# Performance work log

Measured on AMD Instinct MI355X. Metric: run time of the kernel, lower is better.

## Reference

```python
import jax, jax.numpy as jnp
import numpy as np
from jax import lax

B, R, F = 100, 15, 4096       # batch, regions, feature dim
V, E, D, A, T = 10000, 1024, 1024, 512, 500  # vocab, embed, decoder, attention, topic
LIN = 1024                    # autoencoder linear output width
NT = 5                        # sentences per paragraph
L = 52                        # max caption length


def setup_inputs() -> dict:
    key = jax.random.key(0)
    ks = jax.random.split(key, 16)
    g = lambda i, shp, s: jax.random.normal(ks[i], shp, jnp.float32) * s
    return {
        "image_features": g(0, (B, R, F), 1.0),
        "encoded_captions": jax.random.randint(ks[1], (B, NT, L), 0, V),
        "caption_lengths": jax.random.randint(ks[2], (B, NT), 1, L),
        # autoencoder
        "W_lt": g(3, (LIN, F), 0.02), "b_lt": jnp.zeros((LIN,), jnp.float32),
        "conv_w": g(4, (6, 1, 15, 26), 0.05), "conv_b": jnp.zeros((6,), jnp.float32),
        # attention MLP (weight_norm linears == plain linears mathematically)
        "W_feat": g(5, (A, F), 0.02), "b_feat": jnp.zeros((A,), jnp.float32),
        "W_dec": g(6, (A, D), 0.02), "b_dec": jnp.zeros((A,), jnp.float32),
        "W_top": g(7, (A, T), 0.02), "b_top": jnp.zeros((A,), jnp.float32),
        "W_full": g(8, (1, A), 0.02), "b_full": jnp.zeros((1,), jnp.float32),
        # embedding + LSTM cells + output heads
        "emb": g(9, (V, E), 0.1),
        "W_ih1": g(10, (4 * D, E + F + D), 0.01), "W_hh1": g(11, (4 * D, D), 0.01),
        "b_ih1": jnp.zeros((4 * D,), jnp.float32), "b_hh1": jnp.zeros((4 * D,), jnp.float32),
        "W_ih2": g(12, (4 * D, F + D), 0.01), "W_hh2": g(13, (4 * D, D), 0.01),
        "b_ih2": jnp.zeros((4 * D,), jnp.float32), "b_hh2": jnp.zeros((4 * D,), jnp.float32),
        "W_fc1": g(14, (V, D), 0.02), "b_fc1": jnp.zeros((V,), jnp.float32),
        "W_fc": g(15, (V, D), 0.02), "b_fc": jnp.zeros((V,), jnp.float32),
    }


def _lstm_cell(x, h, c, W_ih, W_hh, b_ih, b_hh):
    gates = x @ W_ih.T + b_ih + h @ W_hh.T + b_hh
    i, f, g_, o = jnp.split(gates, 4, axis=-1)
    c = jax.nn.sigmoid(f) * c + jax.nn.sigmoid(i) * jnp.tanh(g_)
    h = jax.nn.sigmoid(o) * jnp.tanh(c)
    return h, c


def reference(image_features, encoded_captions, caption_lengths, W_lt, b_lt,
              conv_w, conv_b, W_feat, b_feat, W_dec, b_dec, W_top, b_top,
              W_full, b_full, emb, W_ih1, W_hh1, b_ih1, b_hh1,
              W_ih2, W_hh2, b_ih2, b_hh2, W_fc1, b_fc1, W_fc, b_fc):
    def per_sample(img, caps, lens):
        # img (R,F), caps (NT,L) int, lens (NT,) int
        img_mean = img.mean(0)  # (F,)
        # autoencoder: linear 4096->1024, conv2d(1->6, k=(15,26), stride 2)
        x = (img @ W_lt.T + b_lt)[None, None]  # (1,1,R,LIN)
        conv = lax.conv_general_dilated(x, conv_w, (2, 2), "VALID",
                                        dimension_numbers=("NCHW", "OIHW", "NCHW"))
        topics = conv[0, :, 0, :] + conv_b[:, None]  # (6, T=500)
        att1 = img @ W_feat.T + b_feat               # (R,A), precomputed once
        # last word of each sentence: caps[t, lens[t]-1]
        last_words = jnp.take_along_axis(caps, (lens - 1)[:, None], axis=1)[:, 0]  # (NT,)
        last_embs = emb[last_words]                  # (NT,E)

        def step(carry, tup):
            h1, c1, h2, c2 = carry
            topic_t, emb_t = tup
            # top-down attention LSTM: cat([h2, img_mean, word_emb])
            x1 = jnp.concatenate([h2, img_mean, emb_t])
            h1, c1 = _lstm_cell(x1, h1, c1, W_ih1, W_hh1, b_ih1, b_hh1)
            # attention over R regions (dropout is identity in eval)
            att = jax.nn.relu(att1 + (h1 @ W_dec.T + b_dec) + (topic_t @ W_top.T + b_top))
            scores = att @ W_full[0] + b_full[0]     # (R,)
            alpha = jax.nn.softmax(scores)
            awe = alpha @ img                        # (F,)
            preds1 = h1 @ W_fc1.T + b_fc1            # (V,)
            h2, c2 = _lstm_cell(jnp.concatenate([awe, h1]), h2, c2,
                                W_ih2, W_hh2, b_ih2, b_hh2)
            preds = h2 @ W_fc.T + b_fc               # (V,)
            return (h1, c1, h2, c2), (preds, preds1)

        z = jnp.zeros((D,), img.dtype)
        _, (preds, preds1) = lax.scan(step, (z, z, z, z), (topics[:NT], last_embs))
        return preds, preds1                          # (NT,V) each

    preds, preds1 = jax.vmap(per_sample)(image_features, encoded_captions, caption_lengths)
    return preds, preds1, encoded_captions, caption_lengths - 1
```

## Files before the change

kernel.cpp:

```cpp
#include <hip/hip_runtime.h>

typedef __attribute__((ext_vector_type(8))) short short8;
typedef __attribute__((ext_vector_type(4))) short short4v;
typedef __attribute__((ext_vector_type(4))) float f32x4;

__device__ __forceinline__ unsigned short f2bf(float f) {
  unsigned int u = __float_as_uint(f);
  u += 0x7fffu + ((u >> 16) & 1u);
  return (unsigned short)(u >> 16);
}
__device__ __forceinline__ float bf2f(unsigned short u) {
  return __uint_as_float(((unsigned int)u) << 16);
}
__device__ __forceinline__ float sigm(float x) { return 1.f / (1.f + expf(-x)); }

template<int NKC>
__global__ __launch_bounds__(256) void gemm_v5(
    const unsigned short* __restrict__ X, int ldx,
    const unsigned short* __restrict__ W, int ldw, int N,
    unsigned short* __restrict__ C, long long slotStride)
{
  __shared__ short8 lds[3584];
  const int tid = threadIdx.x;
  const int lane = tid & 63, wv = tid >> 6;
  const int l16 = lane & 15, kg = (lane >> 4) * 8;
  const int mbase = blockIdx.y * 112;
  const int ncol = blockIdx.x * 64 + wv * 16 + l16;
  const int nrow = (ncol < N) ? ncol : (N - 1);
  const long long k0 = (long long)blockIdx.z * (NKC * 256);
  C += (long long)blockIdx.z * slotStride;

  const unsigned short* wp = W + (size_t)nrow * ldw + kg + k0;
  const unsigned short* xb = X + (size_t)(mbase + l16) * ldx + kg + k0;
  const size_t xrow = (size_t)16 * ldx;

  f32x4 acc[7];
#pragma unroll
  for (int i = 0; i < 7; ++i) acc[i] = (f32x4){0.f, 0.f, 0.f, 0.f};

  for (int kc = 0; kc < NKC; ++kc) {
    if (kc) __syncthreads();
    short8 wbuf[8];
#pragma unroll
    for (int ks = 0; ks < 8; ++ks)
      wbuf[ks] = *(const short8*)(wp + kc * 256 + ks * 32);
    short8 xst[14];
#pragma unroll
    for (int i = 0; i < 14; ++i) {
      const int f = wv + i * 4, mt = f >> 3, ks = f & 7;
      xst[i] = *(const short8*)(xb + (size_t)mt * xrow + kc * 256 + ks * 32);
    }
#pragma unroll
    for (int i = 0; i < 14; ++i) lds[(wv + i * 4) * 64 + lane] = xst[i];
    __syncthreads();
#pragma unroll
    for (int ks = 0; ks < 8; ++ks)
#pragma unroll
      for (int mt = 0; mt < 7; ++mt) {
        short8 a = lds[(mt * 8 + ks) * 64 + lane];
        acc[mt] = __builtin_amdgcn_mfma_f32_16x16x32_bf16(a, wbuf[ks], acc[mt], 0, 0, 0);
      }
  }
  if (ncol < N) {
    const int r0 = (lane >> 4) * 4;
#pragma unroll
    for (int mt = 0; mt < 7; ++mt)
#pragma unroll
      for (int r = 0; r < 4; ++r)
        C[(size_t)(mbase + mt * 16 + r0 + r) * N + ncol] = f2bf(acc[mt][r]);
  }
}

template<int NKC>
__global__ __launch_bounds__(256) void gemm_v5f(
    const unsigned short* __restrict__ X, int ldx,
    const float* __restrict__ W, int ldw, int N,
    unsigned short* __restrict__ C, long long slotStride)
{
  __shared__ short8 lds[3584];
  const int tid = threadIdx.x;
  const int lane = tid & 63, wv = tid >> 6;
  const int l16 = lane & 15, kg = (lane >> 4) * 8;
  const int mbase = blockIdx.y * 112;
  const int ncol = blockIdx.x * 64 + wv * 16 + l16;
  const int nrow = (ncol < N) ? ncol : (N - 1);
  const long long k0 = (long long)blockIdx.z * (NKC * 256);
  C += (long long)blockIdx.z * slotStride;

  const float* wp = W + (size_t)nrow * ldw + kg + k0;
  const unsigned short* xb = X + (size_t)(mbase + l16) * ldx + kg + k0;
  const size_t xrow = (size_t)16 * ldx;

  f32x4 acc[7];
#pragma unroll
  for (int i = 0; i < 7; ++i) acc[i] = (f32x4){0.f, 0.f, 0.f, 0.f};

  for (int kc = 0; kc < NKC; ++kc) {
    if (kc) __syncthreads();
    float4 wa[8], wb[8];
#pragma unroll
    for (int ks = 0; ks < 8; ++ks) {
      wa[ks] = *(const float4*)(wp + kc * 256 + ks * 32);
      wb[ks] = *(const float4*)(wp + kc * 256 + ks * 32 + 4);
    }
    short8 xst[14];
#pragma unroll
    for (int i = 0; i < 14; ++i) {
      const int f = wv + i * 4, mt = f >> 3, ks = f & 7;
      xst[i] = *(const short8*)(xb + (size_t)mt * xrow + kc * 256 + ks * 32);
    }
#pragma unroll
    for (int i = 0; i < 14; ++i) lds[(wv + i * 4) * 64 + lane] = xst[i];
    __syncthreads();
#pragma unroll
    for (int ks = 0; ks < 8; ++ks) {
      short8 w;
      w[0] = (short)f2bf(wa[ks].x); w[1] = (short)f2bf(wa[ks].y);
      w[2] = (short)f2bf(wa[ks].z); w[3] = (short)f2bf(wa[ks].w);
      w[4] = (short)f2bf(wb[ks].x); w[5] = (short)f2bf(wb[ks].y);
      w[6] = (short)f2bf(wb[ks].z); w[7] = (short)f2bf(wb[ks].w);
#pragma unroll
      for (int mt = 0; mt < 7; ++mt) {
        short8 a = lds[(mt * 8 + ks) * 64 + lane];
        acc[mt] = __builtin_amdgcn_mfma_f32_16x16x32_bf16(a, w, acc[mt], 0, 0, 0);
      }
    }
  }
  if (ncol < N) {
    const int r0 = (lane >> 4) * 4;
#pragma unroll
    for (int mt = 0; mt < 7; ++mt)
#pragma unroll
      for (int r = 0; r < 4; ++r)
        C[(size_t)(mbase + mt * 16 + r0 + r) * N + ncol] = f2bf(acc[mt][r]);
  }
}

template<int NKC>
__global__ __launch_bounds__(256) void gemm_dwf(
    const unsigned short* __restrict__ X, int ldx,
    const float* __restrict__ W, int ldw, int N,
    float* __restrict__ outF, const float* __restrict__ bias,
    long long ldc, int rowLim)
{
  __shared__ short8 lds[3584];
  const int tid = threadIdx.x;
  const int lane = tid & 63, wv = tid >> 6;
  const int l16 = lane & 15, kg = (lane >> 4) * 8;
  const int mbase = blockIdx.y * 112;
  const int ncol = blockIdx.x * 64 + wv * 16 + l16;
  const int nrow = (ncol < N) ? ncol : (N - 1);

  const float* wp = W + (size_t)nrow * ldw + kg;
  const unsigned short* xb = X + (size_t)(mbase + l16) * ldx + kg;
  const size_t xrow = (size_t)16 * ldx;

  f32x4 acc[7];
#pragma unroll
  for (int i = 0; i < 7; ++i) acc[i] = (f32x4){0.f, 0.f, 0.f, 0.f};

  for (int kc = 0; kc < NKC; ++kc) {
    if (kc) __syncthreads();
    float4 wa[8], wb[8];
#pragma unroll
    for (int ks = 0; ks < 8; ++ks) {
      wa[ks] = *(const float4*)(wp + kc * 256 + ks * 32);
      wb[ks] = *(const float4*)(wp + kc * 256 + ks * 32 + 4);
    }
    short8 xst[14];
#pragma unroll
    for (int i = 0; i < 14; ++i) {
      const int f = wv + i * 4, mt = f >> 3, ks = f & 7;
      xst[i] = *(const short8*)(xb + (size_t)mt * xrow + kc * 256 + ks * 32);
    }
#pragma unroll
    for (int i = 0; i < 14; ++i) lds[(wv + i * 4) * 64 + lane] = xst[i];
    __syncthreads();
#pragma unroll
    for (int ks = 0; ks < 8; ++ks) {
      short8 w;
      w[0] = (short)f2bf(wa[ks].x); w[1] = (short)f2bf(wa[ks].y);
      w[2] = (short)f2bf(wa[ks].z); w[3] = (short)f2bf(wa[ks].w);
      w[4] = (short)f2bf(wb[ks].x); w[5] = (short)f2bf(wb[ks].y);
      w[6] = (short)f2bf(wb[ks].z); w[7] = (short)f2bf(wb[ks].w);
#pragma unroll
      for (int mt = 0; mt < 7; ++mt) {
        short8 a = lds[(mt * 8 + ks) * 64 + lane];
        acc[mt] = __builtin_amdgcn_mfma_f32_16x16x32_bf16(a, w, acc[mt], 0, 0, 0);
      }
    }
  }
  if (ncol < N) {
    const float bv = bias ? bias[ncol] : 0.f;
    const int r0 = (lane >> 4) * 4;
#pragma unroll
    for (int mt = 0; mt < 7; ++mt)
#pragma unroll
      for (int r = 0; r < 4; ++r) {
        const int row = mbase + mt * 16 + r0 + r;
        if (row < rowLim) outF[(size_t)row * ldc + ncol] = acc[mt][r] + bv;
      }
  }
}

template<int NKC>
__global__ __launch_bounds__(256) void gemm_dwf_split(
    const unsigned short* __restrict__ X, int ldx,
    const float* __restrict__ W1, const float* __restrict__ W2,
    float* __restrict__ outF, const float* __restrict__ bias,
    unsigned short* __restrict__ aux)
{
  __shared__ short8 lds[3584];
  const int tid = threadIdx.x;
  const int lane = tid & 63, wv = tid >> 6;
  const int l16 = lane & 15, kg = (lane >> 4) * 8;
  const int ncol0 = blockIdx.x * 64 + wv * 16 + l16;
  const int ncol = (ncol0 < 10512) ? ncol0 : 10511;
  const float* wp = ((ncol < 10000) ? W1 + (size_t)ncol * 1024
                                    : W2 + (size_t)(ncol - 10000) * 1024) + kg;
  const unsigned short* xb = X + (size_t)l16 * ldx + kg;
  const size_t xrow = (size_t)16 * ldx;

  f32x4 acc[7];
#pragma unroll
  for (int i = 0; i < 7; ++i) acc[i] = (f32x4){0.f, 0.f, 0.f, 0.f};

  for (int kc = 0; kc < NKC; ++kc) {
    if (kc) __syncthreads();
    float4 wa[8], wb[8];
#pragma unroll
    for (int ks = 0; ks < 8; ++ks) {
      wa[ks] = *(const float4*)(wp + kc * 256 + ks * 32);
      wb[ks] = *(const float4*)(wp + kc * 256 + ks * 32 + 4);
    }
    short8 xst[14];
#pragma unroll
    for (int i = 0; i < 14; ++i) {
      const int f = wv + i * 4, mt = f >> 3, ks = f & 7;
      xst[i] = *(const short8*)(xb + (size_t)mt * xrow + kc * 256 + ks * 32);
    }
#pragma unroll
    for (int i = 0; i < 14; ++i) lds[(wv + i * 4) * 64 + lane] = xst[i];
    __syncthreads();
#pragma unroll
    for (int ks = 0; ks < 8; ++ks) {
      short8 w;
      w[0] = (short)f2bf(wa[ks].x); w[1] = (short)f2bf(wa[ks].y);
      w[2] = (short)f2bf(wa[ks].z); w[3] = (short)f2bf(wa[ks].w);
      w[4] = (short)f2bf(wb[ks].x); w[5] = (short)f2bf(wb[ks].y);
      w[6] = (short)f2bf(wb[ks].z); w[7] = (short)f2bf(wb[ks].w);
#pragma unroll
      for (int mt = 0; mt < 7; ++mt) {
        short8 a = lds[(mt * 8 + ks) * 64 + lane];
        acc[mt] = __builtin_amdgcn_mfma_f32_16x16x32_bf16(a, w, acc[mt], 0, 0, 0);
      }
    }
  }
  if (ncol0 < 10000) {
    const float bv = bias[ncol0];
    const int r0 = (lane >> 4) * 4;
#pragma unroll
    for (int mt = 0; mt < 7; ++mt)
#pragma unroll
      for (int r = 0; r < 4; ++r) {
        const int row = mt * 16 + r0 + r;
        if (row < 100) outF[(size_t)row * 50000 + ncol0] = acc[mt][r] + bv;
      }
  } else if (ncol0 < 10512) {
    const int r0 = (lane >> 4) * 4;
#pragma unroll
    for (int mt = 0; mt < 7; ++mt)
#pragma unroll
      for (int r = 0; r < 4; ++r)
        aux[(size_t)(mt * 16 + r0 + r) * 512 + (ncol0 - 10000)] = f2bf(acc[mt][r]);
  }
}

__global__ __launch_bounds__(256) void k_pack_all(
    const float* __restrict__ Wih1, const float* __restrict__ Whh1,
    const float* __restrict__ Wih2, const float* __restrict__ Whh2,
    const float* __restrict__ Wtop,
    unsigned short* __restrict__ Wg1, unsigned short* __restrict__ Wg2,
    unsigned short* __restrict__ Wtopb)
{
  int i = blockIdx.x * 256 + threadIdx.x;
  float4 v; unsigned short* dst; long long di;
  if (i < 2097152) {
    int row = i >> 9, c4 = i & 511;
    const float* s = (c4 < 256) ? Wih1 + (size_t)row * 6144 + c4 * 4
                                : Whh1 + (size_t)row * 1024 + (c4 - 256) * 4;
    v = *(const float4*)s; dst = Wg1; di = i;
  } else if (i < 8388608) {
    int j = i - 2097152; int row = j / 1536, c4 = j - row * 1536;
    const float* s = (c4 < 1280) ? Wih2 + (size_t)row * 5120 + c4 * 4
                                 : Whh2 + (size_t)row * 1024 + (c4 - 1280) * 4;
    v = *(const float4*)s; dst = Wg2; di = j;
  } else {
    int j = i - 8388608; if (j >= 65536) return;
    int n = j >> 7, c4 = j & 127;
    v = (c4 < 125) ? *(const float4*)(Wtop + (size_t)n * 500 + c4 * 4)
                   : (float4){0.f, 0.f, 0.f, 0.f};
    dst = Wtopb; di = j;
  }
  short4v o; o[0] = (short)f2bf(v.x); o[1] = (short)f2bf(v.y);
  o[2] = (short)f2bf(v.z); o[3] = (short)f2bf(v.w);
  ((short4v*)dst)[di] = o;
}

__global__ __launch_bounds__(256) void k_ximg2(const float* __restrict__ img,
    unsigned short* __restrict__ Ximg, unsigned short* __restrict__ Xmean) {
  int idx = blockIdx.x * 256 + threadIdx.x;
  int b = idx >> 12, f = idx & 4095;
  float s = 0.f;
#pragma unroll
  for (int r = 0; r < 15; ++r) {
    float v = img[((size_t)(b * 15 + r) << 12) + f];
    s += v;
    Ximg[((size_t)(b * 15 + r) << 12) + f] = f2bf(v);
  }
  Xmean[((size_t)b << 12) + f] = f2bf(s * (1.f / 15.f));
}

__global__ __launch_bounds__(512) void k_conv(const float* __restrict__ lin,
    const float* __restrict__ cw, const float* __restrict__ cb,
    float* __restrict__ topics) {
  int b = blockIdx.x;
  __shared__ float L[15 * 1024];
  for (int i = threadIdx.x; i < 15 * 1024; i += 512) L[i] = lin[(size_t)b * 15360 + i];
  __syncthreads();
  for (int idx = threadIdx.x; idx < 2500; idx += 512) {
    int tt = idx / 500, w = idx - tt * 500;
    float s = cb[tt];
    for (int kh = 0; kh < 15; ++kh) {
      const float* lr = &L[kh * 1024 + 2 * w];
      const float* wr = &cw[(tt * 15 + kh) * 26];
#pragma unroll
      for (int kw = 0; kw < 26; ++kw) s += lr[kw] * wr[kw];
    }
    topics[(size_t)b * 2500 + idx] = s;
  }
}

__global__ __launch_bounds__(256) void k_padtop(const float* __restrict__ topics,
    unsigned short* __restrict__ Xtop) {
  int idx = blockIdx.x * 256 + threadIdx.x;
  if (idx >= 560 * 512) return;
  int r = idx >> 9, k = idx & 511;
  Xtop[idx] = (r < 500 && k < 500) ? f2bf(topics[(size_t)r * 500 + k]) : (unsigned short)0;
}

__global__ void k_wc(const int* __restrict__ caps, const int* __restrict__ lens,
                     int* __restrict__ words, float* __restrict__ out2,
                     float* __restrict__ out3) {
  int idx = blockIdx.x * 256 + threadIdx.x;
  if (idx < 26000) out2[idx] = (float)caps[idx];
  if (idx < 500) {
    int len = lens[idx];
    words[idx] = caps[idx * 52 + len - 1];
    out3[idx] = (float)(len - 1);
  }
}

__global__ __launch_bounds__(256) void k_gather(const float* __restrict__ emb,
    const int* __restrict__ words, unsigned short* __restrict__ Xemb) {
  int idx = blockIdx.x * 256 + threadIdx.x;
  int bt = idx >> 10, e = idx & 1023;
  Xemb[idx] = (bt < 500) ? f2bf(emb[(size_t)words[bt] * 1024 + e]) : (unsigned short)0;
}

__global__ __launch_bounds__(256) void k_gbase1(const unsigned short* __restrict__ P,
    const float* __restrict__ bih, const float* __restrict__ bhh,
    float* __restrict__ gb) {
  int idx = blockIdx.x * 256 + threadIdx.x;
  int m = idx >> 12, n = idx & 4095;
  float s = bih[n] + bhh[n];
#pragma unroll
  for (int sl = 0; sl < 4; ++sl) s += bf2f(P[((size_t)sl * 112 + m) * 4096 + n]);
  gb[idx] = s;
}

__global__ __launch_bounds__(256) void k_lstm1(const unsigned short* __restrict__ P,
    const float* __restrict__ gb1, const float* __restrict__ gemb, int t,
    float* __restrict__ c1, unsigned short* __restrict__ Xh1,
    unsigned short* __restrict__ X1, unsigned short* __restrict__ X2) {
  int idx = blockIdx.x * 256 + threadIdx.x;
  int b = idx >> 10, j = idx & 1023;
  float g[4];
#pragma unroll
  for (int x = 0; x < 4; ++x) {
    int col = (x << 10) + j;
    float s = gb1[b * 4096 + col] + gemb[((size_t)b * 5 + t) * 4096 + col];
#pragma unroll
    for (int sl = 0; sl < 4; ++sl) s += bf2f(P[((size_t)sl * 112 + b) * 4096 + col]);
    g[x] = s;
  }
  float c = sigm(g[1]) * c1[idx] + sigm(g[0]) * tanhf(g[2]);
  float h = sigm(g[3]) * tanhf(c);
  c1[idx] = c;
  unsigned short hb = f2bf(h);
  Xh1[idx] = hb;
  X1[b * 2048 + 1024 + j] = hb;
  X2[(size_t)b * 6144 + 4096 + j] = hb;
}

__global__ __launch_bounds__(256) void k_attawe(const float* __restrict__ att1,
    const unsigned short* __restrict__ padec, const float* __restrict__ bdec,
    const float* __restrict__ btop, const unsigned short* __restrict__ ttopb,
    const float* __restrict__ wfull, int t,
    const unsigned short* __restrict__ Ximg, unsigned short* __restrict__ X2) {
  int b = blockIdx.x;
  int tid = threadIdx.x;
  int r = tid & 15, ch = tid >> 4;
  __shared__ float sp[16][17];
  __shared__ float al[16];
  float s = 0.f;
  if (r < 15) {
    const float* a1 = att1 + ((size_t)b * 15 + r) * 512;
    const unsigned short* tp = ttopb + ((size_t)b * 5 + t) * 512;
#pragma unroll
    for (int j = 0; j < 32; ++j) {
      int n = ch * 32 + j;
      float ad = bdec[n] + btop[n] + bf2f(padec[(size_t)b * 512 + n]);
      float v = a1[n] + ad + bf2f(tp[n]);
      s += fmaxf(v, 0.f) * wfull[n];
    }
  }
  sp[r][ch] = s;
  __syncthreads();
  if (tid == 0) {
    float sc[15];
    float m = -1e30f;
    for (int rr = 0; rr < 15; ++rr) {
      float x = 0.f;
      for (int cc = 0; cc < 16; ++cc) x += sp[rr][cc];
      sc[rr] = x; m = fmaxf(m, x);
    }
    float sum = 0.f;
    for (int rr = 0; rr < 15; ++rr) { sc[rr] = expf(sc[rr] - m); sum += sc[rr]; }
    float inv = 1.f / sum;
    for (int rr = 0; rr < 15; ++rr) al[rr] = sc[rr] * inv;
  }
  __syncthreads();
  for (int f = tid; f < 4096; f += 256) {
    float s2 = 0.f;
#pragma unroll
    for (int rr = 0; rr < 15; ++rr)
      s2 += al[rr] * bf2f(Ximg[((size_t)b * 15 + rr) * 4096 + f]);
    X2[(size_t)b * 6144 + f] = f2bf(s2);
  }
}

__global__ __launch_bounds__(256) void k_lstm2(const unsigned short* __restrict__ P,
    const float* __restrict__ bih, const float* __restrict__ bhh,
    float* __restrict__ c2, unsigned short* __restrict__ Xh2,
    unsigned short* __restrict__ X1, unsigned short* __restrict__ X2) {
  int idx = blockIdx.x * 256 + threadIdx.x;
  int b = idx >> 10, j = idx & 1023;
  float g[4];
#pragma unroll
  for (int x = 0; x < 4; ++x) {
    int col = (x << 10) + j;
    float s = bih[col] + bhh[col];
#pragma unroll
    for (int sl = 0; sl < 6; ++sl) s += bf2f(P[((size_t)sl * 112 + b) * 4096 + col]);
    g[x] = s;
  }
  float c = sigm(g[1]) * c2[idx] + sigm(g[0]) * tanhf(g[2]);
  float h = sigm(g[3]) * tanhf(c);
  c2[idx] = c;
  unsigned short hb = f2bf(h);
  Xh2[idx] = hb;
  X1[b * 2048 + j] = hb;
  X2[(size_t)b * 6144 + 5120 + j] = hb;
}

extern "C" void kernel_launch(void* const* d_in, const int* in_sizes, int n_in,
                              void* d_out, int out_size, void* d_ws, size_t ws_size,
                              hipStream_t stream) {
  (void)in_sizes; (void)n_in; (void)out_size;
  const float* imgf  = (const float*)d_in[0];
  const int*   caps  = (const int*)d_in[1];
  const int*   lens  = (const int*)d_in[2];
  const float* W_lt  = (const float*)d_in[3];
  const float* b_lt  = (const float*)d_in[4];
  const float* convw = (const float*)d_in[5];
  const float* convb = (const float*)d_in[6];
  const float* W_feat = (const float*)d_in[7];
  const float* b_feat = (const float*)d_in[8];
  const float* W_dec = (const float*)d_in[9];
  const float* b_dec = (const float*)d_in[10];
  const float* W_top = (const float*)d_in[11];
  const float* b_top = (const float*)d_in[12];
  const float* W_full = (const float*)d_in[13];
  const float* b_full = (const float*)d_in[14];  (void)b_full;
  const float* emb   = (const float*)d_in[15];
  const float* W_ih1 = (const float*)d_in[16];
  const float* W_hh1 = (const float*)d_in[17];
  const float* b_ih1 = (const float*)d_in[18];
  const float* b_hh1 = (const float*)d_in[19];
  const float* W_ih2 = (const float*)d_in[20];
  const float* W_hh2 = (const float*)d_in[21];
  const float* b_ih2 = (const float*)d_in[22];
  const float* b_hh2 = (const float*)d_in[23];
  const float* W_fc1 = (const float*)d_in[24];
  const float* b_fc1 = (const float*)d_in[25];
  const float* W_fc  = (const float*)d_in[26];
  const float* b_fc  = (const float*)d_in[27];
  float* out = (float*)d_out;

  char* ws = (char*)d_ws;
  size_t off = 0;
  auto alloc = [&](size_t bytes) -> size_t {
    size_t o = off; off = (off + bytes + 255) & ~(size_t)255; return o;
  };
  const size_t oZERO  = off;
  const size_t oXimg  = alloc(1568ull * 4096 * 2);
  const size_t oXmean = alloc(112ull * 4096 * 2);
  const size_t oX1    = alloc(112ull * 2048 * 2);
  const size_t oX2    = alloc(112ull * 6144 * 2);
  const size_t oXh1   = alloc(112ull * 1024 * 2);
  const size_t oXh2   = alloc(112ull * 1024 * 2);
  const size_t oc1    = alloc(100ull * 1024 * 4);
  const size_t oc2    = alloc(100ull * 1024 * 4);
  const size_t zeroBytes = off - oZERO;
  const size_t oXemb  = alloc(560ull * 1024 * 2);
  const size_t olin   = alloc(1568ull * 1024 * 4);
  const size_t otop   = alloc(100ull * 2500 * 4);
  const size_t oXtop  = alloc(560ull * 512 * 2);
  const size_t oTtopb = alloc(560ull * 512 * 2);
  const size_t oatt1  = alloc(1568ull * 512 * 4);
  const size_t ogb1   = alloc(112ull * 4096 * 4);
  const size_t ogemb  = alloc(560ull * 4096 * 4);
  const size_t owords = alloc(512ull * 4);
  const size_t opg    = alloc(6ull * 112 * 4096 * 2);
  const size_t opadec = alloc(112ull * 512 * 2);
  const size_t oWg1   = alloc(4096ull * 2048 * 2);
  const size_t oWg2   = alloc(4096ull * 6144 * 2);
  const size_t oWtopb = alloc(512ull * 512 * 2);
  if (ws_size < off) return;

  unsigned short* Ximg  = (unsigned short*)(ws + oXimg);
  unsigned short* Xmean = (unsigned short*)(ws + oXmean);
  unsigned short* Xemb  = (unsigned short*)(ws + oXemb);
  unsigned short* X1    = (unsigned short*)(ws + oX1);
  unsigned short* X2    = (unsigned short*)(ws + oX2);
  unsigned short* Xh1   = (unsigned short*)(ws + oXh1);
  unsigned short* Xh2   = (unsigned short*)(ws + oXh2);
  float* c1    = (float*)(ws + oc1);
  float* c2    = (float*)(ws + oc2);
  float* lin   = (float*)(ws + olin);
  float* topics = (float*)(ws + otop);
  unsigned short* Xtop  = (unsigned short*)(ws + oXtop);
  unsigned short* Ttopb = (unsigned short*)(ws + oTtopb);
  float* att1  = (float*)(ws + oatt1);
  float* gb1   = (float*)(ws + ogb1);
  float* gemb  = (float*)(ws + ogemb);
  int*   words = (int*)(ws + owords);
  unsigned short* pg    = (unsigned short*)(ws + opg);
  unsigned short* padec = (unsigned short*)(ws + opadec);
  unsigned short* Wg1   = (unsigned short*)(ws + oWg1);
  unsigned short* Wg2   = (unsigned short*)(ws + oWg2);
  unsigned short* Wtopb = (unsigned short*)(ws + oWtopb);

  const long long S4 = 112ll * 4096;

  hipMemsetAsync(ws + oZERO, 0, zeroBytes, stream);

  k_ximg2<<<1600, 256, 0, stream>>>(imgf, Ximg, Xmean);
  k_pack_all<<<33024, 256, 0, stream>>>(W_ih1, W_hh1, W_ih2, W_hh2, W_top,
                                        Wg1, Wg2, Wtopb);
  gemm_dwf<16><<<dim3(16, 14, 1), 256, 0, stream>>>(Ximg, 4096, W_lt, 4096, 1024,
                                                    lin, b_lt, 1024, 1568);
  k_conv<<<100, 512, 0, stream>>>(lin, convw, convb, topics);
  k_padtop<<<1120, 256, 0, stream>>>(topics, Xtop);
  gemm_v5<2><<<dim3(8, 5, 1), 256, 0, stream>>>(Xtop, 512, Wtopb, 512, 512, Ttopb, 0);
  gemm_dwf<16><<<dim3(8, 14, 1), 256, 0, stream>>>(Ximg, 4096, W_feat, 4096, 512,
                                                   att1, b_feat, 512, 1568);
  k_wc<<<102, 256, 0, stream>>>(caps, lens, words, out + 10000000, out + 10026000);
  k_gather<<<2240, 256, 0, stream>>>(emb, words, Xemb);
  gemm_v5f<4><<<dim3(64, 1, 4), 256, 0, stream>>>(Xmean, 4096, W_ih1 + 1024, 6144, 4096,
                                                  pg, S4);
  k_gbase1<<<1792, 256, 0, stream>>>(pg, b_ih1, b_hh1, gb1);
  gemm_dwf<4><<<dim3(64, 5, 1), 256, 0, stream>>>(Xemb, 1024, W_ih1 + 5120, 6144, 4096,
                                                  gemb, nullptr, 4096, 560);

  for (int t = 0; t < 5; ++t) {
    gemm_v5<2><<<dim3(64, 1, 4), 256, 0, stream>>>(X1, 2048, Wg1, 2048, 4096, pg, S4);
    k_lstm1<<<400, 256, 0, stream>>>(pg, gb1, gemb, t, c1, Xh1, X1, X2);
    gemm_dwf_split<4><<<dim3(165, 1, 1), 256, 0, stream>>>(
        Xh1, 1024, W_fc1, W_dec, out + 5000000 + t * 10000, b_fc1, padec);
    k_attawe<<<100, 256, 0, stream>>>(att1, padec, b_dec, b_top, Ttopb, W_full, t,
                                      Ximg, X2);
    gemm_v5<4><<<dim3(64, 1, 6), 256, 0, stream>>>(X2, 6144, Wg2, 6144, 4096, pg, S4);
    k_lstm2<<<400, 256, 0, stream>>>(pg, b_ih2, b_hh2, c2, Xh2, X1, X2);
    gemm_dwf<4><<<dim3(157, 1, 1), 256, 0, stream>>>(Xh2, 1024, W_fc, 1024, 10000,
                                                     out + t * 10000, b_fc, 50000, 100);
  }
}
```

Baseline: 789.2 us.

## Double-buffer GEMMs with direct global-to-LDS loads, prepack fc weights to bf16, split-K prologue

Replaces all GEMM kernels with double-buffered variants that use global_load_lds to stage X and W tiles into shared memory, overlapping the next chunk's loads with MFMA compute. W_fc1/W_dec and W_fc are pre-packed to bf16 once so the per-step output heads read half the bytes and skip per-element conversion. Prologue GEMMs (W_lt, W_feat) move to split-K with bf16 partials plus a reduce kernel, and several small kernels (padtop, wc/gather) are fused into conv and a new gather kernel. This adds extra packing traffic and larger LDS usage, which may reduce occupancy, and split-K partials in bf16 add rounding.

```diff
diff --git a/kernel.cpp b/kernel.cpp
--- a/kernel.cpp
+++ b/kernel.cpp
@@ -14,251 +14,245 @@
 }
 __device__ __forceinline__ float sigm(float x) { return 1.f / (1.f + expf(-x)); }
 
-template<int NKC>
-__global__ __launch_bounds__(256) void gemm_v5(
+typedef const __attribute__((address_space(1))) unsigned int GUI;
+typedef __attribute__((address_space(3))) unsigned int LUI;
+__device__ __forceinline__ void g2l16(const void* g, void* l) {
+  __builtin_amdgcn_global_load_lds((GUI*)g, (LUI*)l, 16, 0, 0);
+}
+template<int N> __device__ __forceinline__ void waitvm() {
+  if constexpr (N == 0)       asm volatile("s_waitcnt vmcnt(0)" ::: "memory");
+  else if constexpr (N == 11) asm volatile("s_waitcnt vmcnt(11)" ::: "memory");
+  else                        asm volatile("s_waitcnt vmcnt(15)" ::: "memory");
+}
+
+template<int NCH, bool OUTF32>
+__global__ __launch_bounds__(256) void gemm_pb(
     const unsigned short* __restrict__ X, int ldx,
     const unsigned short* __restrict__ W, int ldw, int N,
-    unsigned short* __restrict__ C, long long slotStride)
+    void* __restrict__ Cv, long long slotStride,
+    const float* __restrict__ bias, long long ldc, int rowLim)
 {
-  __shared__ short8 lds[3584];
-  const int tid = threadIdx.x;
-  const int lane = tid & 63, wv = tid >> 6;
+  __shared__ __align__(16) char smem[2 * 28672 + 2 * 16384];
+  const int tid = threadIdx.x, lane = tid & 63, wv = tid >> 6;
   const int l16 = lane & 15, kg = (lane >> 4) * 8;
   const int mbase = blockIdx.y * 112;
   const int ncol = blockIdx.x * 64 + wv * 16 + l16;
   const int nrow = (ncol < N) ? ncol : (N - 1);
-  const long long k0 = (long long)blockIdx.z * (NKC * 256);
-  C += (long long)blockIdx.z * slotStride;
-
-  const unsigned short* wp = W + (size_t)nrow * ldw + kg + k0;
-  const unsigned short* xb = X + (size_t)(mbase + l16) * ldx + kg + k0;
-  const size_t xrow = (size_t)16 * ldx;
+  const long long kbase = (long long)blockIdx.z * (NCH * 128);
+
+  const unsigned short* xb = X + (size_t)(mbase + l16) * ldx + kbase + kg;
+  const unsigned short* wb = W + (size_t)nrow * ldw + kbase + kg;
+  const size_t xrow16 = (size_t)16 * ldx;
+
+  auto stage = [&](int nb, int ch) {
+#pragma unroll
+    for (int i = 0; i < 7; ++i) {
+      const int f = wv + i * 4, mt = f >> 2, ks = f & 3;
+      g2l16(xb + (size_t)mt * xrow16 + ch * 128 + ks * 32,
+            smem + nb * 28672 + f * 1024);
+    }
+#pragma unroll
+    for (int ks = 0; ks < 4; ++ks)
+      g2l16(wb + ch * 128 + ks * 32,
+            smem + 57344 + nb * 16384 + (wv * 4 + ks) * 1024);
+  };
 
   f32x4 acc[7];
 #pragma unroll
   for (int i = 0; i < 7; ++i) acc[i] = (f32x4){0.f, 0.f, 0.f, 0.f};
 
-  for (int kc = 0; kc < NKC; ++kc) {
-    if (kc) __syncthreads();
-    short8 wbuf[8];
-#pragma unroll
-    for (int ks = 0; ks < 8; ++ks)
-      wbuf[ks] = *(const short8*)(wp + kc * 256 + ks * 32);
-    short8 xst[14];
-#pragma unroll
-    for (int i = 0; i < 14; ++i) {
-      const int f = wv + i * 4, mt = f >> 3, ks = f & 7;
-      xst[i] = *(const short8*)(xb + (size_t)mt * xrow + kc * 256 + ks * 32);
-    }
-#pragma unroll
-    for (int i = 0; i < 14; ++i) lds[(wv + i * 4) * 64 + lane] = xst[i];
-    __syncthreads();
-#pragma unroll
-    for (int ks = 0; ks < 8; ++ks)
+  stage(0, 0);
+#pragma unroll
+  for (int t = 0; t < NCH; ++t) {
+    if (t + 1 < NCH) { stage((t + 1) & 1, t + 1); waitvm<11>(); }
+    else waitvm<0>();
+    __builtin_amdgcn_s_barrier();
+    __builtin_amdgcn_sched_barrier(0);
+    const char* xs  = smem + (t & 1) * 28672;
+    const char* wsm = smem + 57344 + (t & 1) * 16384;
+#pragma unroll
+    for (int ks = 0; ks < 4; ++ks) {
+      short8 w = *(const short8*)(wsm + (wv * 4 + ks) * 1024 + lane * 16);
 #pragma unroll
       for (int mt = 0; mt < 7; ++mt) {
-        short8 a = lds[(mt * 8 + ks) * 64 + lane];
-        acc[mt] = __builtin_amdgcn_mfma_f32_16x16x32_bf16(a, wbuf[ks], acc[mt], 0, 0, 0);
+        short8 a = *(const short8*)(xs + (mt * 4 + ks) * 1024 + lane * 16);
+        acc[mt] = __builtin_amdgcn_mfma_f32_16x16x32_bf16(a, w, acc[mt], 0, 0, 0);
       }
-  }
+    }
+    __builtin_amdgcn_sched_barrier(0);
+    __builtin_amdgcn_s_barrier();
+  }
+
   if (ncol < N) {
     const int r0 = (lane >> 4) * 4;
-#pragma unroll
-    for (int mt = 0; mt < 7; ++mt)
-#pragma unroll
-      for (int r = 0; r < 4; ++r)
-        C[(size_t)(mbase + mt * 16 + r0 + r) * N + ncol] = f2bf(acc[mt][r]);
-  }
-}
-
-template<int NKC>
-__global__ __launch_bounds__(256) void gemm_v5f(
+    if constexpr (OUTF32) {
+      float* outF = (float*)Cv;
+      const float bv = bias ? bias[ncol] : 0.f;
+#pragma unroll
+      for (int mt = 0; mt < 7; ++mt)
+#pragma unroll
+        for (int r = 0; r < 4; ++r) {
+          const int row = mbase + mt * 16 + r0 + r;
+          if (row < rowLim) outF[(size_t)row * ldc + ncol] = acc[mt][r] + bv;
+        }
+    } else {
+      unsigned short* C = (unsigned short*)Cv + (long long)blockIdx.z * slotStride;
+#pragma unroll
+      for (int mt = 0; mt < 7; ++mt)
+#pragma unroll
+        for (int r = 0; r < 4; ++r)
+          C[(size_t)(mbase + mt * 16 + r0 + r) * N + ncol] = f2bf(acc[mt][r]);
+    }
+  }
+}
+
+template<int NCH, bool OUTF32>
+__global__ __launch_bounds__(256) void gemm_pf(
     const unsigned short* __restrict__ X, int ldx,
     const float* __restrict__ W, int ldw, int N,
-    unsigned short* __restrict__ C, long long slotStride)
+    void* __restrict__ Cv, long long slotStride,
+    const float* __restrict__ bias, long long ldc, int rowLim)
 {
-  __shared__ short8 lds[3584];
-  const int tid = threadIdx.x;
-  const int lane = tid & 63, wv = tid >> 6;
+  __shared__ __align__(16) char smem[2 * 28672 + 2 * 32768];
+  const int tid = threadIdx.x, lane = tid & 63, wv = tid >> 6;
   const int l16 = lane & 15, kg = (lane >> 4) * 8;
   const int mbase = blockIdx.y * 112;
   const int ncol = blockIdx.x * 64 + wv * 16 + l16;
   const int nrow = (ncol < N) ? ncol : (N - 1);
-  const long long k0 = (long long)blockIdx.z * (NKC * 256);
-  C += (long long)blockIdx.z * slotStride;
-
-  const float* wp = W + (size_t)nrow * ldw + kg + k0;
-  const unsigned short* xb = X + (size_t)(mbase + l16) * ldx + kg + k0;
-  const size_t xrow = (size_t)16 * ldx;
+  const long long kbase = (long long)blockIdx.z * (NCH * 128);
+
+  const unsigned short* xb = X + (size_t)(mbase + l16) * ldx + kbase + kg;
+  const float* wb = W + (size_t)nrow * ldw + kbase + kg;
+  const size_t xrow16 = (size_t)16 * ldx;
+
+  auto stage = [&](int nb, int ch) {
+#pragma unroll
+    for (int i = 0; i < 7; ++i) {
+      const int f = wv + i * 4, mt = f >> 2, ks = f & 3;
+      g2l16(xb + (size_t)mt * xrow16 + ch * 128 + ks * 32,
+            smem + nb * 28672 + f * 1024);
+    }
+#pragma unroll
+    for (int ks = 0; ks < 4; ++ks)
+#pragma unroll
+      for (int h = 0; h < 2; ++h)
+        g2l16(wb + ch * 128 + ks * 32 + h * 4,
+              smem + 57344 + nb * 32768 + ((wv * 4 + ks) * 2 + h) * 1024);
+  };
 
   f32x4 acc[7];
 #pragma unroll
   for (int i = 0; i < 7; ++i) acc[i] = (f32x4){0.f, 0.f, 0.f, 0.f};
 
-  for (int kc = 0; kc < NKC; ++kc) {
-    if (kc) __syncthreads();
-    float4 wa[8], wb[8];
-#pragma unroll
-    for (int ks = 0; ks < 8; ++ks) {
-      wa[ks] = *(const float4*)(wp + kc * 256 + ks * 32);
-      wb[ks] = *(const float4*)(wp + kc * 256 + ks * 32 + 4);
-    }
-    short8 xst[14];
-#pragma unroll
-    for (int i = 0; i < 14; ++i) {
-      const int f = wv + i * 4, mt = f >> 3, ks = f & 7;
-      xst[i] = *(const short8*)(xb + (size_t)mt * xrow + kc * 256 + ks * 32);
-    }
-#pragma unroll
-    for (int i = 0; i < 14; ++i) lds[(wv + i * 4) * 64 + lane] = xst[i];
-    __syncthreads();
-#pragma unroll
-    for (int ks = 0; ks < 8; ++ks) {
+  stage(0, 0);
+#pragma unroll
+  for (int t = 0; t < NCH; ++t) {
+    if (t + 1 < NCH) { stage((t + 1) & 1, t + 1); waitvm<15>(); }
+    else waitvm<0>();
+    __builtin_amdgcn_s_barrier();
+    __builtin_amdgcn_sched_barrier(0);
+    const char* xs  = smem + (t & 1) * 28672;
+    const char* wsm = smem + 57344 + (t & 1) * 32768;
+#pragma unroll
+    for (int ks = 0; ks < 4; ++ks) {
+      float4 wa = *(const float4*)(wsm + ((wv * 4 + ks) * 2 + 0) * 1024 + lane * 16);
+      float4 wc = *(const float4*)(wsm + ((wv * 4 + ks) * 2 + 1) * 1024 + lane * 16);
       short8 w;
-      w[0] = (short)f2bf(wa[ks].x); w[1] = (short)f2bf(wa[ks].y);
-      w[2] = (short)f2bf(wa[ks].z); w[3] = (short)f2bf(wa[ks].w);
-      w[4] = (short)f2bf(wb[ks].x); w[5] = (short)f2bf(wb[ks].y);
-      w[6] = (short)f2bf(wb[ks].z); w[7] = (short)f2bf(wb[ks].w);
+      w[0] = (short)f2bf(wa.x); w[1] = (short)f2bf(wa.y);
+      w[2] = (short)f2bf(wa.z); w[3] = (short)f2bf(wa.w);
+      w[4] = (short)f2bf(wc.x); w[5] = (short)f2bf(wc.y);
+      w[6] = (short)f2bf(wc.z); w[7] = (short)f2bf(wc.w);
 #pragma unroll
       for (int mt = 0; mt < 7; ++mt) {
-        short8 a = lds[(mt * 8 + ks) * 64 + lane];
+        short8 a = *(const short8*)(xs + (mt * 4 + ks) * 1024 + lane * 16);
         acc[mt] = __builtin_amdgcn_mfma_f32_16x16x32_bf16(a, w, acc[mt], 0, 0, 0);
       }
     }
-  }
+    __builtin_amdgcn_sched_barrier(0);
+    __builtin_amdgcn_s_barrier();
+  }
+
   if (ncol < N) {
     const int r0 = (lane >> 4) * 4;
-#pragma unroll
-    for (int mt = 0; mt < 7; ++mt)
-#pragma unroll
-      for (int r = 0; r < 4; ++r)
-        C[(size_t)(mbase + mt * 16 + r0 + r) * N + ncol] = f2bf(acc[mt][r]);
-  }
-}
-
-template<int NKC>
-__global__ __launch_bounds__(256) void gemm_dwf(
-    const unsigned short* __restrict__ X, int ldx,
-    const float* __restrict__ W, int ldw, int N,
+    if constexpr (OUTF32) {
+      float* outF = (float*)Cv;
+      const float bv = bias ? bias[ncol] : 0.f;
+#pragma unroll
+      for (int mt = 0; mt < 7; ++mt)
+#pragma unroll
+        for (int r = 0; r < 4; ++r) {
+          const int row = mbase + mt * 16 + r0 + r;
+          if (row < rowLim) outF[(size_t)row * ldc + ncol] = acc[mt][r] + bv;
+        }
+    } else {
+      unsigned short* C = (unsigned short*)Cv + (long long)blockIdx.z * slotStride;
+#pragma unroll
+      for (int mt = 0; mt < 7; ++mt)
+#pragma unroll
+        for (int r = 0; r < 4; ++r)
+          C[(size_t)(mbase + mt * 16 + r0 + r) * N + ncol] = f2bf(acc[mt][r]);
+    }
+  }
+}
+
+__global__ __launch_bounds__(256) void gemm_pcat(
+    const unsigned short* __restrict__ X,
+    const unsigned short* __restrict__ W,
     float* __restrict__ outF, const float* __restrict__ bias,
-    long long ldc, int rowLim)
+    unsigned short* __restrict__ padec)
 {
-  __shared__ short8 lds[3584];
-  const int tid = threadIdx.x;
-  const int lane = tid & 63, wv = tid >> 6;
+  __shared__ __align__(16) char smem[2 * 28672 + 2 * 16384];
+  const int tid = threadIdx.x, lane = tid & 63, wv = tid >> 6;
   const int l16 = lane & 15, kg = (lane >> 4) * 8;
-  const int mbase = blockIdx.y * 112;
-  const int ncol = blockIdx.x * 64 + wv * 16 + l16;
-  const int nrow = (ncol < N) ? ncol : (N - 1);
-
-  const float* wp = W + (size_t)nrow * ldw + kg;
-  const unsigned short* xb = X + (size_t)(mbase + l16) * ldx + kg;
-  const size_t xrow = (size_t)16 * ldx;
+  const int ncol0 = blockIdx.x * 64 + wv * 16 + l16;
+  const int nrow = (ncol0 < 10512) ? ncol0 : 10511;
+
+  const unsigned short* xb = X + (size_t)l16 * 1024 + kg;
+  const unsigned short* wb = W + (size_t)nrow * 1024 + kg;
+  const size_t xrow16 = (size_t)16 * 1024;
+
+  auto stage = [&](int nb, int ch) {
+#pragma unroll
+    for (int i = 0; i < 7; ++i) {
+      const int f = wv + i * 4, mt = f >> 2, ks = f & 3;
+      g2l16(xb + (size_t)mt * xrow16 + ch * 128 + ks * 32,
+            smem + nb * 28672 + f * 1024);
+    }
+#pragma unroll
+    for (int ks = 0; ks < 4; ++ks)
+      g2l16(wb + ch * 128 + ks * 32,
+            smem + 57344 + nb * 16384 + (wv * 4 + ks) * 1024);
+  };
 
   f32x4 acc[7];
 #pragma unroll
   for (int i = 0; i < 7; ++i) acc[i] = (f32x4){0.f, 0.f, 0.f, 0.f};
 
-  for (int kc = 0; kc < NKC; ++kc) {
-    if (kc) __syncthreads();
-    float4 wa[8], wb[8];
-#pragma unroll
-    for (int ks = 0; ks < 8; ++ks) {
-      wa[ks] = *(const float4*)(wp + kc * 256 + ks * 32);
-      wb[ks] = *(const float4*)(wp + kc * 256 + ks * 32 + 4);
-    }
-    short8 xst[14];
-#pragma unroll
-    for (int i = 0; i < 14; ++i) {
-      const int f = wv + i * 4, mt = f >> 3, ks = f & 7;
-      xst[i] = *(const short8*)(xb + (size_t)mt * xrow + kc * 256 + ks * 32);
-    }
-#pragma unroll
-    for (int i = 0; i < 14; ++i) lds[(wv + i * 4) * 64 + lane] = xst[i];
-    __syncthreads();
-#pragma unroll
-    for (int ks = 0; ks < 8; ++ks) {
-      short8 w;
-      w[0] = (short)f2bf(wa[ks].x); w[1] = (short)f2bf(wa[ks].y);
-      w[2] = (short)f2bf(wa[ks].z); w[3] = (short)f2bf(wa[ks].w);
-      w[4] = (short)f2bf(wb[ks].x); w[5] = (short)f2bf(wb[ks].y);
-      w[6] = (short)f2bf(wb[ks].z); w[7] = (short)f2bf(wb[ks].w);
+  stage(0, 0);
+#pragma unroll
+  for (int t = 0; t < 8; ++t) {
+    if (t + 1 < 8) { stage((t + 1) & 1, t + 1); waitvm<11>(); }
+    else waitvm<0>();
+    __builtin_amdgcn_s_barrier();
+    __builtin_amdgcn_sched_barrier(0);
+    const char* xs  = smem + (t & 1) * 28672;
+    const char* wsm = smem + 57344 + (t & 1) * 16384;
+#pragma unroll
+    for (int ks = 0; ks < 4; ++ks) {
+      short8 w = *(const short8*)(wsm + (wv * 4 + ks) * 1024 + lane * 16);
 #pragma unroll
       for (int mt = 0; mt < 7; ++mt) {
-        short8 a = lds[(mt * 8 + ks) * 64 + lane];
+        short8 a = *(const short8*)(xs + (mt * 4 + ks) * 1024 + lane * 16);
         acc[mt] = __builtin_amdgcn_mfma_f32_16x16x32_bf16(a, w, acc[mt], 0, 0, 0);
       }
     }
-  }
-  if (ncol < N) {
-    const float bv = bias ? bias[ncol] : 0.f;
-    const int r0 = (lane >> 4) * 4;
-#pragma unroll
-    for (int mt = 0; mt < 7; ++mt)
-#pragma unroll
-      for (int r = 0; r < 4; ++r) {
-        const int row = mbase + mt * 16 + r0 + r;
-        if (row < rowLim) outF[(size_t)row * ldc + ncol] = acc[mt][r] + bv;
-      }
-  }
-}
-
-template<int NKC>
-__global__ __launch_bounds__(256) void gemm_dwf_split(
-    const unsigned short* __restrict__ X, int ldx,
-    const float* __restrict__ W1, const float* __restrict__ W2,
-    float* __restrict__ outF, const float* __restrict__ bias,
-    unsigned short* __restrict__ aux)
-{
-  __shared__ short8 lds[3584];
-  const int tid = threadIdx.x;
-  const int lane = tid & 63, wv = tid >> 6;
-  const int l16 = lane & 15, kg = (lane >> 4) * 8;
-  const int ncol0 = blockIdx.x * 64 + wv * 16 + l16;
-  const int ncol = (ncol0 < 10512) ? ncol0 : 10511;
-  const float* wp = ((ncol < 10000) ? W1 + (size_t)ncol * 1024
-                                    : W2 + (size_t)(ncol - 10000) * 1024) + kg;
-  const unsigned short* xb = X + (size_t)l16 * ldx + kg;
-  const size_t xrow = (size_t)16 * ldx;
-
-  f32x4 acc[7];
-#pragma unroll
-  for (int i = 0; i < 7; ++i) acc[i] = (f32x4){0.f, 0.f, 0.f, 0.f};
-
-  for (int kc = 0; kc < NKC; ++kc) {
-    if (kc) __syncthreads();
-    float4 wa[8], wb[8];
-#pragma unroll
-    for (int ks = 0; ks < 8; ++ks) {
-      wa[ks] = *(const float4*)(wp + kc * 256 + ks * 32);
-      wb[ks] = *(const float4*)(wp + kc * 256 + ks * 32 + 4);
-    }
-    short8 xst[14];
-#pragma unroll
-    for (int i = 0; i < 14; ++i) {
-      const int f = wv + i * 4, mt = f >> 3, ks = f & 7;
-      xst[i] = *(const short8*)(xb + (size_t)mt * xrow + kc * 256 + ks * 32);
-    }
-#pragma unroll
-    for (int i = 0; i < 14; ++i) lds[(wv + i * 4) * 64 + lane] = xst[i];
-    __syncthreads();
-#pragma unroll
-    for (int ks = 0; ks < 8; ++ks) {
-      short8 w;
-      w[0] = (short)f2bf(wa[ks].x); w[1] = (short)f2bf(wa[ks].y);
-      w[2] = (short)f2bf(wa[ks].z); w[3] = (short)f2bf(wa[ks].w);
-      w[4] = (short)f2bf(wb[ks].x); w[5] = (short)f2bf(wb[ks].y);
-      w[6] = (short)f2bf(wb[ks].z); w[7] = (short)f2bf(wb[ks].w);
-#pragma unroll
-      for (int mt = 0; mt < 7; ++mt) {
-        short8 a = lds[(mt * 8 + ks) * 64 + lane];
-        acc[mt] = __builtin_amdgcn_mfma_f32_16x16x32_bf16(a, w, acc[mt], 0, 0, 0);
-      }
-    }
-  }
+    __builtin_amdgcn_sched_barrier(0);
+    __builtin_amdgcn_s_barrier();
+  }
+
+  const int r0 = (lane >> 4) * 4;
   if (ncol0 < 10000) {
     const float bv = bias[ncol0];
-    const int r0 = (lane >> 4) * 4;
 #pragma unroll
     for (int mt = 0; mt < 7; ++mt)
 #pragma unroll
@@ -267,20 +261,21 @@
         if (row < 100) outF[(size_t)row * 50000 + ncol0] = acc[mt][r] + bv;
       }
   } else if (ncol0 < 10512) {
-    const int r0 = (lane >> 4) * 4;
 #pragma unroll
     for (int mt = 0; mt < 7; ++mt)
 #pragma unroll
       for (int r = 0; r < 4; ++r)
-        aux[(size_t)(mt * 16 + r0 + r) * 512 + (ncol0 - 10000)] = f2bf(acc[mt][r]);
+        padec[(size_t)(mt * 16 + r0 + r) * 512 + (ncol0 - 10000)] = f2bf(acc[mt][r]);
   }
 }
 
 __global__ __launch_bounds__(256) void k_pack_all(
     const float* __restrict__ Wih1, const float* __restrict__ Whh1,
     const float* __restrict__ Wih2, const float* __restrict__ Whh2,
-    const float* __restrict__ Wtop,
+    const float* __restrict__ Wfc1, const float* __restrict__ Wdec,
+    const float* __restrict__ Wfc,  const float* __restrict__ Wtop,
     unsigned short* __restrict__ Wg1, unsigned short* __restrict__ Wg2,
+    unsigned short* __restrict__ Wcat, unsigned short* __restrict__ Wfcb,
     unsigned short* __restrict__ Wtopb)
 {
   int i = blockIdx.x * 256 + threadIdx.x;
@@ -295,8 +290,14 @@
     const float* s = (c4 < 1280) ? Wih2 + (size_t)row * 5120 + c4 * 4
                                  : Whh2 + (size_t)row * 1024 + (c4 - 1280) * 4;
     v = *(const float4*)s; dst = Wg2; di = j;
-  } else {
-    int j = i - 8388608; if (j >= 65536) return;
+  } else if (i < 11079680) {
+    int j = i - 8388608; int row = j >> 8, c4 = j & 255;
+    const float* s = (row < 10000) ? Wfc1 + (size_t)row * 1024 + c4 * 4
+                                   : Wdec + (size_t)(row - 10000) * 1024 + c4 * 4;
+    v = *(const float4*)s; dst = Wcat; di = j;
+  } else if (i < 13639680) { int j = i - 11079680; v = ((const float4*)Wfc)[j]; dst = Wfcb; di = j; }
+  else {
+    int j = i - 13639680; if (j >= 65536) return;
     int n = j >> 7, c4 = j & 127;
     v = (c4 < 125) ? *(const float4*)(Wtop + (size_t)n * 500 + c4 * 4)
                    : (float4){0.f, 0.f, 0.f, 0.f};
@@ -321,12 +322,28 @@
   Xmean[((size_t)b << 12) + f] = f2bf(s * (1.f / 15.f));
 }
 
-__global__ __launch_bounds__(512) void k_conv(const float* __restrict__ lin,
-    const float* __restrict__ cw, const float* __restrict__ cb,
-    float* __restrict__ topics) {
+__global__ __launch_bounds__(256) void k_reduce(const unsigned short* __restrict__ P,
+    long long ss, int nslots, const float* __restrict__ bias, int colmask,
+    float* __restrict__ out, int total) {
+  int idx = blockIdx.x * 256 + threadIdx.x;
+  if (idx >= total) return;
+  float s = bias ? bias[idx & colmask] : 0.f;
+  for (int sl = 0; sl < nslots; ++sl) s += bf2f(P[(size_t)sl * ss + idx]);
+  out[idx] = s;
+}
+
+__global__ __launch_bounds__(512) void k_conv(const unsigned short* __restrict__ px,
+    const float* __restrict__ blt, const float* __restrict__ cw,
+    const float* __restrict__ cb, unsigned short* __restrict__ Xtop) {
   int b = blockIdx.x;
   __shared__ float L[15 * 1024];
-  for (int i = threadIdx.x; i < 15 * 1024; i += 512) L[i] = lin[(size_t)b * 15360 + i];
+  for (int i = threadIdx.x; i < 15 * 1024; i += 512) {
+    float s = blt[i & 1023];
+#pragma unroll
+    for (int sl = 0; sl < 2; ++sl)
+      s += bf2f(px[(size_t)sl * 1605632 + (size_t)b * 15360 + i]);
+    L[i] = s;
+  }
   __syncthreads();
   for (int idx = threadIdx.x; idx < 2500; idx += 512) {
     int tt = idx / 500, w = idx - tt * 500;
@@ -337,35 +354,22 @@
 #pragma unroll
       for (int kw = 0; kw < 26; ++kw) s += lr[kw] * wr[kw];
     }
-    topics[(size_t)b * 2500 + idx] = s;
-  }
-}
-
-__global__ __launch_bounds__(256) void k_padtop(const float* __restrict__ topics,
-    unsigned short* __restrict__ Xtop) {
-  int idx = blockIdx.x * 256 + threadIdx.x;
-  if (idx >= 560 * 512) return;
-  int r = idx >> 9, k = idx & 511;
-  Xtop[idx] = (r < 500 && k < 500) ? f2bf(topics[(size_t)r * 500 + k]) : (unsigned short)0;
-}
-
-__global__ void k_wc(const int* __restrict__ caps, const int* __restrict__ lens,
-                     int* __restrict__ words, float* __restrict__ out2,
-                     float* __restrict__ out3) {
-  int idx = blockIdx.x * 256 + threadIdx.x;
-  if (idx < 26000) out2[idx] = (float)caps[idx];
-  if (idx < 500) {
-    int len = lens[idx];
-    words[idx] = caps[idx * 52 + len - 1];
-    out3[idx] = (float)(len - 1);
-  }
-}
-
-__global__ __launch_bounds__(256) void k_gather(const float* __restrict__ emb,
-    const int* __restrict__ words, unsigned short* __restrict__ Xemb) {
+    Xtop[((size_t)(b * 5 + tt)) * 512 + w] = f2bf(s);
+  }
+}
+
+__global__ __launch_bounds__(256) void k_gw(const int* __restrict__ caps,
+    const int* __restrict__ lens, const float* __restrict__ emb,
+    unsigned short* __restrict__ Xemb, float* __restrict__ out2,
+    float* __restrict__ out3) {
   int idx = blockIdx.x * 256 + threadIdx.x;
   int bt = idx >> 10, e = idx & 1023;
-  Xemb[idx] = (bt < 500) ? f2bf(emb[(size_t)words[bt] * 1024 + e]) : (unsigned short)0;
+  if (bt < 500) {
+    int w = caps[bt * 52 + lens[bt] - 1];
+    Xemb[idx] = f2bf(emb[(size_t)w * 1024 + e]);
+  } else if (bt < 560) Xemb[idx] = 0;
+  if (idx < 26000) out2[idx] = (float)caps[idx];
+  if (idx < 500) out3[idx] = (float)(lens[idx] - 1);
 }
 
 __global__ __launch_bounds__(256) void k_gbase1(const unsigned short* __restrict__ P,
@@ -522,20 +526,20 @@
   const size_t oXh2   = alloc(112ull * 1024 * 2);
   const size_t oc1    = alloc(100ull * 1024 * 4);
   const size_t oc2    = alloc(100ull * 1024 * 4);
+  const size_t oXtop  = alloc(560ull * 512 * 2);
   const size_t zeroBytes = off - oZERO;
   const size_t oXemb  = alloc(560ull * 1024 * 2);
-  const size_t olin   = alloc(1568ull * 1024 * 4);
-  const size_t otop   = alloc(100ull * 2500 * 4);
-  const size_t oXtop  = alloc(560ull * 512 * 2);
   const size_t oTtopb = alloc(560ull * 512 * 2);
   const size_t oatt1  = alloc(1568ull * 512 * 4);
   const size_t ogb1   = alloc(112ull * 4096 * 4);
   const size_t ogemb  = alloc(560ull * 4096 * 4);
-  const size_t owords = alloc(512ull * 4);
   const size_t opg    = alloc(6ull * 112 * 4096 * 2);
+  const size_t opx    = alloc(2ull * 1568 * 1024 * 2);
   const size_t opadec = alloc(112ull * 512 * 2);
   const size_t oWg1   = alloc(4096ull * 2048 * 2);
   const size_t oWg2   = alloc(4096ull * 6144 * 2);
+  const size_t oWcat  = alloc(10512ull * 1024 * 2);
+  const size_t oWfcb  = alloc(10000ull * 1024 * 2);
   const size_t oWtopb = alloc(512ull * 512 * 2);
   if (ws_size < off) return;
 
@@ -548,18 +552,18 @@
   unsigned short* Xh2   = (unsigned short*)(ws + oXh2);
   float* c1    = (float*)(ws + oc1);
   float* c2    = (float*)(ws + oc2);
-  float* lin   = (float*)(ws + olin);
-  float* topics = (float*)(ws + otop);
   unsigned short* Xtop  = (unsigned short*)(ws + oXtop);
   unsigned short* Ttopb = (unsigned short*)(ws + oTtopb);
   float* att1  = (float*)(ws + oatt1);
   float* gb1   = (float*)(ws + ogb1);
   float* gemb  = (float*)(ws + ogemb);
-  int*   words = (int*)(ws + owords);
   unsigned short* pg    = (unsigned short*)(ws + opg);
+  unsigned short* px    = (unsigned short*)(ws + opx);
   unsigned short* padec = (unsigned short*)(ws + opadec);
   unsigned short* Wg1   = (unsigned short*)(ws + oWg1);
   unsigned short* Wg2   = (unsigned short*)(ws + oWg2);
+  unsigned short* Wcat  = (unsigned short*)(ws + oWcat);
+  unsigned short* Wfcb  = (unsigned short*)(ws + oWfcb);
   unsigned short* Wtopb = (unsigned short*)(ws + oWtopb);
 
   const long long S4 = 112ll * 4096;
@@ -567,33 +571,35 @@
   hipMemsetAsync(ws + oZERO, 0, zeroBytes, stream);
 
   k_ximg2<<<1600, 256, 0, stream>>>(imgf, Ximg, Xmean);
-  k_pack_all<<<33024, 256, 0, stream>>>(W_ih1, W_hh1, W_ih2, W_hh2, W_top,
-                                        Wg1, Wg2, Wtopb);
-  gemm_dwf<16><<<dim3(16, 14, 1), 256, 0, stream>>>(Ximg, 4096, W_lt, 4096, 1024,
-                                                    lin, b_lt, 1024, 1568);
-  k_conv<<<100, 512, 0, stream>>>(lin, convw, convb, topics);
-  k_padtop<<<1120, 256, 0, stream>>>(topics, Xtop);
-  gemm_v5<2><<<dim3(8, 5, 1), 256, 0, stream>>>(Xtop, 512, Wtopb, 512, 512, Ttopb, 0);
-  gemm_dwf<16><<<dim3(8, 14, 1), 256, 0, stream>>>(Ximg, 4096, W_feat, 4096, 512,
-                                                   att1, b_feat, 512, 1568);
-  k_wc<<<102, 256, 0, stream>>>(caps, lens, words, out + 10000000, out + 10026000);
-  k_gather<<<2240, 256, 0, stream>>>(emb, words, Xemb);
-  gemm_v5f<4><<<dim3(64, 1, 4), 256, 0, stream>>>(Xmean, 4096, W_ih1 + 1024, 6144, 4096,
-                                                  pg, S4);
+  k_pack_all<<<53536, 256, 0, stream>>>(W_ih1, W_hh1, W_ih2, W_hh2, W_fc1, W_dec,
+                                        W_fc, W_top, Wg1, Wg2, Wcat, Wfcb, Wtopb);
+  gemm_pf<16, false><<<dim3(16, 14, 2), 256, 0, stream>>>(
+      Ximg, 4096, W_lt, 4096, 1024, px, 1568ll * 1024, nullptr, 0, 0);
+  k_conv<<<100, 512, 0, stream>>>(px, b_lt, convw, convb, Xtop);
+  gemm_pb<4, false><<<dim3(8, 5, 1), 256, 0, stream>>>(
+      Xtop, 512, Wtopb, 512, 512, Ttopb, 0, nullptr, 0, 0);
+  gemm_pf<8, false><<<dim3(8, 14, 4), 256, 0, stream>>>(
+      Ximg, 4096, W_feat, 4096, 512, px, 1568ll * 512, nullptr, 0, 0);
+  k_reduce<<<3136, 256, 0, stream>>>(px, 1568ll * 512, 4, b_feat, 511, att1, 1568 * 512);
+  k_gw<<<2240, 256, 0, stream>>>(caps, lens, emb, Xemb, out + 10000000, out + 10026000);
+  gemm_pf<8, false><<<dim3(64, 1, 4), 256, 0, stream>>>(
+      Xmean, 4096, W_ih1 + 1024, 6144, 4096, pg, S4, nullptr, 0, 0);
   k_gbase1<<<1792, 256, 0, stream>>>(pg, b_ih1, b_hh1, gb1);
-  gemm_dwf<4><<<dim3(64, 5, 1), 256, 0, stream>>>(Xemb, 1024, W_ih1 + 5120, 6144, 4096,
-                                                  gemb, nullptr, 4096, 560);
+  gemm_pf<8, true><<<dim3(64, 5, 1), 256, 0, stream>>>(
+      Xemb, 1024, W_ih1 + 5120, 6144, 4096, gemb, 0, nullptr, 4096, 560);
 
   for (int t = 0; t < 5; ++t) {
-    gemm_v5<2><<<dim3(64, 1, 4), 256, 0, stream>>>(X1, 2048, Wg1, 2048, 4096, pg, S4);
+    gemm_pb<4, false><<<dim3(64, 1, 4), 256, 0, stream>>>(
+        X1, 2048, Wg1, 2048, 4096, pg, S4, nullptr, 0, 0);
     k_lstm1<<<400, 256, 0, stream>>>(pg, gb1, gemb, t, c1, Xh1, X1, X2);
-    gemm_dwf_split<4><<<dim3(165, 1, 1), 256, 0, stream>>>(
-        Xh1, 1024, W_fc1, W_dec, out + 5000000 + t * 10000, b_fc1, padec);
+    gemm_pcat<<<dim3(165, 1, 1), 256, 0, stream>>>(
+        Xh1, Wcat, out + 5000000 + t * 10000, b_fc1, padec);
     k_attawe<<<100, 256, 0, stream>>>(att1, padec, b_dec, b_top, Ttopb, W_full, t,
                                       Ximg, X2);
-    gemm_v5<4><<<dim3(64, 1, 6), 256, 0, stream>>>(X2, 6144, Wg2, 6144, 4096, pg, S4);
+    gemm_pb<8, false><<<dim3(64, 1, 6), 256, 0, stream>>>(
+        X2, 6144, Wg2, 6144, 4096, pg, S4, nullptr, 0, 0);
     k_lstm2<<<400, 256, 0, stream>>>(pg, b_ih2, b_hh2, c2, Xh2, X1, X2);
-    gemm_dwf<4><<<dim3(157, 1, 1), 256, 0, stream>>>(Xh2, 1024, W_fc, 1024, 10000,
-                                                     out + t * 10000, b_fc, 50000, 100);
-  }
-}
+    gemm_pb<8, true><<<dim3(157, 1, 1), 256, 0, stream>>>(
+        Xh2, 1024, Wfcb, 1024, 10000, out + t * 10000, 0, b_fc, 50000, 100);
+  }
+}
```

Measured after the change: 941.1 us. +19.2%, slower.
